# Performance work log

Measured on AMD Instinct MI355X. Metric: run time of the kernel, lower is better.

The kernel has to match this reference:

```python
import jax, jax.numpy as jnp
import numpy as np

N, E = 40000, 640000
IN_DIM, EDGE_DIM, HID = 128, 64, 128


def setup_inputs() -> dict:
    key = jax.random.key(0)
    ks = jax.random.split(key, 10)
    x = jax.random.normal(ks[0], (N, IN_DIM), dtype=jnp.float32)
    edge_index = jax.random.randint(ks[1], (2, E), 0, N, dtype=jnp.int64)
    edge_attr = jax.random.normal(ks[2], (E, EDGE_DIM), dtype=jnp.float32)
    # learned params (xavier-ish scaling)
    Wh_w = jax.random.normal(ks[3], (EDGE_DIM, HID), dtype=jnp.float32) / np.sqrt(EDGE_DIM)
    Wh_b = jnp.zeros((HID,), dtype=jnp.float32)
    Wn_w = jax.random.normal(ks[4], (2 * IN_DIM, HID), dtype=jnp.float32) / np.sqrt(2 * IN_DIM)
    Wn_b = jnp.zeros((HID,), dtype=jnp.float32)
    w_e = jax.random.normal(ks[5], (HID, 1), dtype=jnp.float32) / np.sqrt(HID)
    ft_w = jax.random.normal(ks[6], (IN_DIM, IN_DIM), dtype=jnp.float32) / np.sqrt(IN_DIM)
    ft_b = jnp.zeros((IN_DIM,), dtype=jnp.float32)
    return {"x": x, "edge_index": edge_index, "edge_attr": edge_attr,
            "Wh_w": Wh_w, "Wh_b": Wh_b, "Wn_w": Wn_w, "Wn_b": Wn_b,
            "w_e": w_e, "ft_w": ft_w, "ft_b": ft_b}


def reference(x, edge_index, edge_attr, Wh_w, Wh_b, Wn_w, Wn_b, w_e, ft_w, ft_b):
    src, dst = edge_index[0], edge_index[1]
    # gather endpoint features and run edge MLP: relu(W_h(e) + W_n([x_src; x_dst]))
    node_feat = jnp.concatenate([x[src], x[dst]], axis=1)          # [E, 2*in_dim]
    edge_h = edge_attr @ Wh_w + Wh_b                               # [E, hid]
    node_h = node_feat @ Wn_w + Wn_b                               # [E, hid]
    combined = jax.nn.relu(edge_h + node_h)
    scores = (combined @ w_e)[:, 0]                                # [E]
    alpha = jax.nn.softmax(scores, axis=0)                         # softmax over all edges
    # scatter-add weighted dst features into src nodes (same-type branch)
    local = jnp.zeros_like(x).at[src].add(-alpha[:, None] * x[dst])
    out = x + local
    out = out + out @ ft_w + ft_b
    return out
```

## Files before the change

### kernel.cpp

```cpp
#include <hip/hip_runtime.h>
#include <math.h>

#define N_NODES 40000
#define E_EDGES 640000
#define IN_DIM 128
#define EDGE_DIM 64
#define HID 128
#define EB 10000

typedef unsigned int u32;
typedef unsigned short u16;
typedef __attribute__((ext_vector_type(4))) float f32x4;
typedef __attribute__((ext_vector_type(8))) short bf16x8;

__device__ __forceinline__ float bf_lo(u32 d) { return __uint_as_float(d << 16); }
__device__ __forceinline__ float bf_hi(u32 d) { return __uint_as_float(d & 0xffff0000u); }
__device__ __forceinline__ u16 f2bf(float f) {
    u32 u = __float_as_uint(f);
    return (u16)((u + 0x7fffu + ((u >> 16) & 1u)) >> 16);
}
__device__ __forceinline__ u32 pack_bf(float lo, float hi) {
    return ((u32)f2bf(hi) << 16) | (u32)f2bf(lo);
}


__global__ __launch_bounds__(256) void k_init(const float* __restrict__ x,
                                              u16* __restrict__ xb,
                                              u32* __restrict__ counts) {
    int i = blockIdx.x * 256 + threadIdx.x;
    xb[i] = f2bf(x[i]);
    if (i < N_NODES) counts[i] = 0;
}

__global__ __launch_bounds__(256) void k_trans(const float* __restrict__ Whw,
                                               const float* __restrict__ Wnw,
                                               const float* __restrict__ ftw,
                                               u16* __restrict__ Whtb,
                                               u16* __restrict__ WnAT,
                                               u16* __restrict__ WnBT,
                                               u16* __restrict__ fttb) {
    int i = blockIdx.x * 256 + threadIdx.x;
    if (i < 8192) {
        int h = i >> 6, k = i & 63;
        Whtb[i] = f2bf(Whw[k * HID + h]);
    } else if (i < 24576) {
        int j = i - 8192, h = j >> 7, k = j & 127;
        WnAT[j] = f2bf(Wnw[k * HID + h]);
    } else if (i < 40960) {
        int j = i - 24576, h = j >> 7, k = j & 127;
        WnBT[j] = f2bf(Wnw[(IN_DIM + k) * HID + h]);
    } else {
        int j = i - 40960, h = j >> 7, k = j & 127;
        fttb[j] = f2bf(ftw[k * IN_DIM + h]);
    }
}

__global__ __launch_bounds__(256) void k_proj(const u16* __restrict__ xb,
                                              const u16* __restrict__ WnAT,
                                              const u16* __restrict__ WnBT,
                                              const float* __restrict__ Whb,
                                              const float* __restrict__ Wnb,
                                              u16* __restrict__ P1b,
                                              u16* __restrict__ P2b) {
    const int t = threadIdx.x, w = t >> 6, lane = t & 63;
    const int mrow = lane & 15, quad = lane >> 4;
    const int rowBase = blockIdx.x * 64 + w * 16;

    bf16x8 a[4];
    const u16* ar = xb + (size_t)(rowBase + mrow) * IN_DIM + quad * 8;
#pragma unroll
    for (int ks = 0; ks < 4; ++ks) a[ks] = *(const bf16x8*)(ar + ks * 32);

#pragma unroll
    for (int nt = 0; nt < 8; ++nt) {
        const u16* b1p = WnAT + (size_t)(nt * 16 + mrow) * IN_DIM + quad * 8;
        const u16* b2p = WnBT + (size_t)(nt * 16 + mrow) * IN_DIM + quad * 8;
        f32x4 c1 = {0.f, 0.f, 0.f, 0.f}, c2 = {0.f, 0.f, 0.f, 0.f};
#pragma unroll
        for (int ks = 0; ks < 4; ++ks) {
            c1 = __builtin_amdgcn_mfma_f32_16x16x32_bf16(a[ks], *(const bf16x8*)(b1p + ks * 32), c1, 0, 0, 0);
            c2 = __builtin_amdgcn_mfma_f32_16x16x32_bf16(a[ks], *(const bf16x8*)(b2p + ks * 32), c2, 0, 0, 0);
        }
        const int col = nt * 16 + mrow;
        const float bias = Whb[col] + Wnb[col];
#pragma unroll
        for (int r = 0; r < 4; ++r) {
            int row = rowBase + quad * 4 + r;
            P1b[(size_t)row * HID + col] = f2bf(c1[r] + bias);
            P2b[(size_t)row * HID + col] = f2bf(c2[r]);
        }
    }
}

__global__ __launch_bounds__(256) void k_hist(const int* __restrict__ eidx,
                                              u32* __restrict__ counts) {
    int e = blockIdx.x * 256 + threadIdx.x;
    atomicAdd(&counts[eidx[e]], 1u);
}

__global__ __launch_bounds__(1024) void k_scan(const u32* __restrict__ counts,
                                               u32* __restrict__ off,
                                               u32* __restrict__ cur) {
    __shared__ u32 sums[1024];
    const int t = threadIdx.x;
    const int CH = 40;
    u32 local[CH];
    u32 s = 0;
    const int base = t * CH;
#pragma unroll
    for (int i = 0; i < CH; ++i) {
        int idx = base + i;
        u32 c = (idx < N_NODES) ? counts[idx] : 0u;
        local[i] = s;
        s += c;
    }
    sums[t] = s;
    __syncthreads();
    for (int o = 1; o < 1024; o <<= 1) {
        u32 v = (t >= o) ? sums[t - o] : 0u;
        __syncthreads();
        sums[t] += v;
        __syncthreads();
    }
    const u32 pre = sums[t] - s;
#pragma unroll
    for (int i = 0; i < CH; ++i) {
        int idx = base + i;
        if (idx < N_NODES) {
            u32 v = pre + local[i];
            off[idx] = v;
            cur[idx] = v;
        }
    }
    if (t == 1023) off[N_NODES] = sums[1023];
}

__global__ __launch_bounds__(256) void k_edge(const int* __restrict__ eidx,
                                              const float* __restrict__ ea,
                                              const u16* __restrict__ Whtb,
                                              const u16* __restrict__ P1b,
                                              const u16* __restrict__ P2b,
                                              const float* __restrict__ we,
                                              float* __restrict__ expS,
                                              float* __restrict__ partials) {
    __shared__ u32 Psp[64][68];
    __shared__ float wsumLds[4];
    const int e0 = blockIdx.x * 64;
    const int t = threadIdx.x;

    {
        const int m = t >> 2, c4 = t & 3;
        int src = eidx[e0 + m];
        int dst = eidx[E_EDGES + e0 + m];
        const uint4* p1 = (const uint4*)(P1b + (size_t)src * HID + c4 * 32);
        const uint4* p2 = (const uint4*)(P2b + (size_t)dst * HID + c4 * 32);
#pragma unroll
        for (int i = 0; i < 4; ++i) {
            uint4 ua = p1[i], ub = p2[i];
            u32 da[4] = {ua.x, ua.y, ua.z, ua.w};
            u32 db[4] = {ub.x, ub.y, ub.z, ub.w};
            uint4 o;
            o.x = pack_bf(bf_lo(da[0]) + bf_lo(db[0]), bf_hi(da[0]) + bf_hi(db[0]));
            o.y = pack_bf(bf_lo(da[1]) + bf_lo(db[1]), bf_hi(da[1]) + bf_hi(db[1]));
            o.z = pack_bf(bf_lo(da[2]) + bf_lo(db[2]), bf_hi(da[2]) + bf_hi(db[2]));
            o.w = pack_bf(bf_lo(da[3]) + bf_lo(db[3]), bf_hi(da[3]) + bf_hi(db[3]));
            *(uint4*)&Psp[m][c4 * 16 + i * 4] = o;
        }
    }
    __syncthreads();

    const int w = t >> 6, lane = t & 63;
    const int mrow = lane & 15, quad = lane >> 4;
    const int mt = w;

    const float* arow = ea + (size_t)(e0 + mt * 16 + mrow) * EDGE_DIM + quad * 8;
    bf16x8 a0, a1;
#pragma unroll
    for (int ks = 0; ks < 2; ++ks) {
        float4 f0 = *(const float4*)(arow + ks * 32);
        float4 f1 = *(const float4*)(arow + ks * 32 + 4);
        bf16x8& af = ks ? a1 : a0;
        af[0] = (short)f2bf(f0.x); af[1] = (short)f2bf(f0.y);
        af[2] = (short)f2bf(f0.z); af[3] = (short)f2bf(f0.w);
        af[4] = (short)f2bf(f1.x); af[5] = (short)f2bf(f1.y);
        af[6] = (short)f2bf(f1.z); af[7] = (short)f2bf(f1.w);
    }

    float wsum[4] = {0.f, 0.f, 0.f, 0.f};
    const u16* bbase = Whtb + (size_t)mrow * EDGE_DIM + quad * 8;
#pragma unroll
    for (int nt = 0; nt < 8; ++nt) {
        const u16* bp = bbase + nt * 16 * EDGE_DIM;
        bf16x8 b0 = *(const bf16x8*)(bp);
        bf16x8 b1 = *(const bf16x8*)(bp + 32);
        f32x4 c = {0.f, 0.f, 0.f, 0.f};
        c = __builtin_amdgcn_mfma_f32_16x16x32_bf16(a0, b0, c, 0, 0, 0);
        c = __builtin_amdgcn_mfma_f32_16x16x32_bf16(a1, b1, c, 0, 0, 0);
        float wv = we[nt * 16 + mrow];
#pragma unroll
        for (int r = 0; r < 4; ++r) {
            u32 u = Psp[mt * 16 + quad * 4 + r][nt * 8 + (mrow >> 1)];
            float p = (mrow & 1) ? bf_hi(u) : bf_lo(u);
            wsum[r] += fmaxf(c[r] + p, 0.f) * wv;
        }
    }

#pragma unroll
    for (int off = 1; off < 16; off <<= 1) {
#pragma unroll
        for (int r = 0; r < 4; ++r) wsum[r] += __shfl_xor(wsum[r], off, 16);
    }
    float ex[4]; float s4 = 0.f;
#pragma unroll
    for (int r = 0; r < 4; ++r) { ex[r] = __expf(wsum[r]); s4 += ex[r]; }
    if (mrow == 0) {
#pragma unroll
        for (int r = 0; r < 4; ++r) expS[e0 + mt * 16 + quad * 4 + r] = ex[r];
    }
    s4 += __shfl_xor(s4, 16, 64);
    s4 += __shfl_xor(s4, 32, 64);
    if (lane == 0) wsumLds[w] = s4;
    __syncthreads();
    if (t == 0) partials[blockIdx.x] = wsumLds[0] + wsumLds[1] + wsumLds[2] + wsumLds[3];
}

__global__ __launch_bounds__(256) void k_sum(const float* __restrict__ partials,
                                             float* __restrict__ sumExp) {
    float s = 0.f;
    for (int i = threadIdx.x; i < EB; i += 256) s += partials[i];
#pragma unroll
    for (int off = 1; off < 64; off <<= 1) s += __shfl_xor(s, off, 64);
    __shared__ float ws4[4];
    if ((threadIdx.x & 63) == 0) ws4[threadIdx.x >> 6] = s;
    __syncthreads();
    if (threadIdx.x == 0) sumExp[0] = ws4[0] + ws4[1] + ws4[2] + ws4[3];
}

__global__ __launch_bounds__(256) void k_fill(const int* __restrict__ eidx,
                                              const float* __restrict__ expS,
                                              const float* __restrict__ sumExp,
                                              u32* __restrict__ cur,
                                              u32* __restrict__ sdst,
                                              float* __restrict__ sa) {
    const float invS = 1.0f / sumExp[0];
    int e = blockIdx.x * 256 + threadIdx.x;
    int src = eidx[e];
    int dst = eidx[E_EDGES + e];
    u32 pos = atomicAdd(&cur[src], 1u);
    sdst[pos] = (u32)dst;
    sa[pos]   = -expS[e] * invS;
}

__global__ __launch_bounds__(256) void k_accum(const u32* __restrict__ off,
                                               const u32* __restrict__ sdst,
                                               const float* __restrict__ sa,
                                               const u16* __restrict__ xb,
                                               float* __restrict__ out) {
    const int lane = threadIdx.x & 63;
    const int n = blockIdx.x * 4 + (threadIdx.x >> 6);
    const u32 o0 = off[n], o1 = off[n + 1];

    float acc0 = 0.f, acc1 = 0.f;
    for (u32 base = o0; base < o1; base += 64) {
        u32 j = base + (u32)lane;
        u32 dv = 0; float av = 0.f;
        if (j < o1) { dv = sdst[j]; av = sa[j]; }
        int cnt = (int)min(64u, o1 - base);
        for (int jj = 0; jj < cnt; ++jj) {
            u32 dst = __shfl(dv, jj, 64);
            float a = __shfl(av, jj, 64);
            u32 d = ((const u32*)(xb + (size_t)dst * IN_DIM))[lane];
            acc0 = fmaf(a, bf_lo(d), acc0);
            acc1 = fmaf(a, bf_hi(d), acc1);
        }
    }
    float* op = out + (size_t)n * IN_DIM + 2 * lane;
    op[0] = acc0;
    op[1] = acc1;
}

__global__ __launch_bounds__(256) void k_final(const float* __restrict__ x,
                                               const u16* __restrict__ fttb,
                                               const float* __restrict__ ftb,
                                               float* __restrict__ out) {
    __shared__ u32 ybp[64][68];
    const int t = threadIdx.x;
    const int rb = blockIdx.x * 64;

    {
        const int rr = t >> 2, seg = t & 3;
        const float4* xp = (const float4*)(x + (size_t)(rb + rr) * IN_DIM + seg * 32);
        const float4* lp = (const float4*)(out + (size_t)(rb + rr) * IN_DIM + seg * 32);
#pragma unroll
        for (int i = 0; i < 4; ++i) {
            float4 xa = xp[2 * i], xc = xp[2 * i + 1];
            float4 la = lp[2 * i], lc = lp[2 * i + 1];
            uint4 o;
            o.x = pack_bf(xa.x + la.x, xa.y + la.y);
            o.y = pack_bf(xa.z + la.z, xa.w + la.w);
            o.z = pack_bf(xc.x + lc.x, xc.y + lc.y);
            o.w = pack_bf(xc.z + lc.z, xc.w + lc.w);
            *(uint4*)&ybp[rr][seg * 16 + i * 4] = o;
        }
    }
    __syncthreads();

    const int w = t >> 6, lane = t & 63;
    const int mrow = lane & 15, quad = lane >> 4;
    const int rowBase = rb + w * 16;

    bf16x8 a[4];
#pragma unroll
    for (int ks = 0; ks < 4; ++ks)
        a[ks] = *(const bf16x8*)&ybp[w * 16 + mrow][ks * 16 + quad * 4];

#pragma unroll
    for (int nt = 0; nt < 8; ++nt) {
        const u16* bp = fttb + (size_t)(nt * 16 + mrow) * IN_DIM + quad * 8;
        f32x4 c = {0.f, 0.f, 0.f, 0.f};
#pragma unroll
        for (int ks = 0; ks < 4; ++ks)
            c = __builtin_amdgcn_mfma_f32_16x16x32_bf16(a[ks], *(const bf16x8*)(bp + ks * 32), c, 0, 0, 0);
        const int col = nt * 16 + mrow;
        const float fb = ftb[col];
#pragma unroll
        for (int r = 0; r < 4; ++r) {
            int row = rowBase + quad * 4 + r;
            size_t idx = (size_t)row * IN_DIM + col;
            float y = x[idx] + out[idx];
            out[idx] = y + c[r] + fb;
        }
    }
}

extern "C" void kernel_launch(void* const* d_in, const int* in_sizes, int n_in,
                              void* d_out, int out_size, void* d_ws, size_t ws_size,
                              hipStream_t stream) {
    const float* x    = (const float*)d_in[0];
    const int*   eidx = (const int*)d_in[1];
    const float* ea   = (const float*)d_in[2];
    const float* Whw  = (const float*)d_in[3];
    const float* Whb  = (const float*)d_in[4];
    const float* Wnw  = (const float*)d_in[5];
    const float* Wnb  = (const float*)d_in[6];
    const float* we   = (const float*)d_in[7];
    const float* ftw  = (const float*)d_in[8];
    const float* ftb  = (const float*)d_in[9];
    float* out = (float*)d_out;

    u16*   P1b      = (u16*)d_ws;
    u16*   P2b      = P1b + (size_t)N_NODES * HID;
    u16*   xb       = P2b + (size_t)N_NODES * HID;
    u16*   Whtb     = xb + (size_t)N_NODES * IN_DIM;
    u16*   WnAT     = Whtb + (size_t)EDGE_DIM * HID;
    u16*   WnBT     = WnAT + (size_t)HID * IN_DIM;
    u16*   fttb     = WnBT + (size_t)HID * IN_DIM;
    float* expS     = (float*)(fttb + (size_t)IN_DIM * IN_DIM);
    float* partials = expS + (size_t)E_EDGES;
    float* sumExp   = partials + EB;
    u32*   counts   = (u32*)(sumExp + 1);
    u32*   off      = counts + N_NODES;
    u32*   cur      = off + N_NODES + 1;
    u32*   sdst     = cur + N_NODES;
    float* sa       = (float*)(sdst + E_EDGES);

    k_init <<<(N_NODES * IN_DIM) / 256, 256, 0, stream>>>(x, xb, counts);
    k_trans<<<224, 256, 0, stream>>>(Whw, Wnw, ftw, Whtb, WnAT, WnBT, fttb);
    k_proj <<<N_NODES / 64, 256, 0, stream>>>(xb, WnAT, WnBT, Whb, Wnb, P1b, P2b);
    k_hist <<<E_EDGES / 256, 256, 0, stream>>>(eidx, counts);
    k_scan <<<1, 1024, 0, stream>>>(counts, off, cur);
    k_edge <<<EB, 256, 0, stream>>>(eidx, ea, Whtb, P1b, P2b, we, expS, partials);
    k_sum  <<<1, 256, 0, stream>>>(partials, sumExp);
    k_fill <<<E_EDGES / 256, 256, 0, stream>>>(eidx, expS, sumExp, cur, sdst, sa);
    k_accum<<<N_NODES / 4, 256, 0, stream>>>(off, sdst, sa, xb, out);
    k_final<<<N_NODES / 64, 256, 0, stream>>>(x, fttb, ftb, out);
}
```

Measured before the change: 570.3 us.

## Fuse CSR fill into edge kernel and defer softmax normalization to accumulation

The CSR bucket fill (atomic slot reservation plus writing dst and the unnormalized negative exp score) moves into the edge-score kernel, and the separate fill kernel and expS buffer are removed. Normalization by the global exp sum is applied once per output element in the accumulation kernel. The edge kernel drops its block-wide syncs by giving each wave its own LDS tile and per-wave partial sums, and it issues the gathers and edge_attr loads together before computing. The accumulation loop is unrolled by four with packed (dst, weight) pairs so that more gathers are in flight. In exchange, atomics now run inside the MFMA kernel, which may serialize on hot nodes and add latency there.

```diff
diff --git a/kernel.cpp b/kernel.cpp
--- a/kernel.cpp
+++ b/kernel.cpp
@@ -7,6 +7,7 @@
 #define EDGE_DIM 64
 #define HID 128
 #define EB 10000
+#define NPART (EB * 4)
 
 typedef unsigned int u32;
 typedef unsigned short u16;
@@ -141,50 +142,50 @@
                                               const u16* __restrict__ P1b,
                                               const u16* __restrict__ P2b,
                                               const float* __restrict__ we,
-                                              float* __restrict__ expS,
+                                              u32* __restrict__ cur,
+                                              uint2* __restrict__ sde,
                                               float* __restrict__ partials) {
-    __shared__ u32 Psp[64][68];
-    __shared__ float wsumLds[4];
-    const int e0 = blockIdx.x * 64;
-    const int t = threadIdx.x;
-
-    {
-        const int m = t >> 2, c4 = t & 3;
-        int src = eidx[e0 + m];
-        int dst = eidx[E_EDGES + e0 + m];
-        const uint4* p1 = (const uint4*)(P1b + (size_t)src * HID + c4 * 32);
-        const uint4* p2 = (const uint4*)(P2b + (size_t)dst * HID + c4 * 32);
-#pragma unroll
-        for (int i = 0; i < 4; ++i) {
-            uint4 ua = p1[i], ub = p2[i];
-            u32 da[4] = {ua.x, ua.y, ua.z, ua.w};
-            u32 db[4] = {ub.x, ub.y, ub.z, ub.w};
-            uint4 o;
-            o.x = pack_bf(bf_lo(da[0]) + bf_lo(db[0]), bf_hi(da[0]) + bf_hi(db[0]));
-            o.y = pack_bf(bf_lo(da[1]) + bf_lo(db[1]), bf_hi(da[1]) + bf_hi(db[1]));
-            o.z = pack_bf(bf_lo(da[2]) + bf_lo(db[2]), bf_hi(da[2]) + bf_hi(db[2]));
-            o.w = pack_bf(bf_lo(da[3]) + bf_lo(db[3]), bf_hi(da[3]) + bf_hi(db[3]));
-            *(uint4*)&Psp[m][c4 * 16 + i * 4] = o;
-        }
-    }
-    __syncthreads();
-
-    const int w = t >> 6, lane = t & 63;
+    __shared__ u32 Psp[4][16][68];
+    const int t = threadIdx.x, w = t >> 6, lane = t & 63;
+    const int e0 = blockIdx.x * 64 + w * 16;
     const int mrow = lane & 15, quad = lane >> 4;
-    const int mt = w;
-
-    const float* arow = ea + (size_t)(e0 + mt * 16 + mrow) * EDGE_DIM + quad * 8;
+
+    const int m = lane >> 2, c4 = lane & 3;
+    const int srcm = eidx[e0 + m];
+    const int dstm = eidx[E_EDGES + e0 + m];
+    const uint4* p1 = (const uint4*)(P1b + (size_t)srcm * HID + c4 * 32);
+    const uint4* p2 = (const uint4*)(P2b + (size_t)dstm * HID + c4 * 32);
+    uint4 pa[4], pb[4];
+#pragma unroll
+    for (int i = 0; i < 4; ++i) { pa[i] = p1[i]; pb[i] = p2[i]; }
+
+    const float* arow = ea + (size_t)(e0 + mrow) * EDGE_DIM + quad * 8;
+    float4 f0 = *(const float4*)(arow);
+    float4 f1 = *(const float4*)(arow + 4);
+    float4 f2 = *(const float4*)(arow + 32);
+    float4 f3 = *(const float4*)(arow + 36);
+
+#pragma unroll
+    for (int i = 0; i < 4; ++i) {
+        u32 da[4] = {pa[i].x, pa[i].y, pa[i].z, pa[i].w};
+        u32 db[4] = {pb[i].x, pb[i].y, pb[i].z, pb[i].w};
+        uint4 o;
+        o.x = pack_bf(bf_lo(da[0]) + bf_lo(db[0]), bf_hi(da[0]) + bf_hi(db[0]));
+        o.y = pack_bf(bf_lo(da[1]) + bf_lo(db[1]), bf_hi(da[1]) + bf_hi(db[1]));
+        o.z = pack_bf(bf_lo(da[2]) + bf_lo(db[2]), bf_hi(da[2]) + bf_hi(db[2]));
+        o.w = pack_bf(bf_lo(da[3]) + bf_lo(db[3]), bf_hi(da[3]) + bf_hi(db[3]));
+        *(uint4*)&Psp[w][m][c4 * 16 + i * 4] = o;
+    }
+
     bf16x8 a0, a1;
-#pragma unroll
-    for (int ks = 0; ks < 2; ++ks) {
-        float4 f0 = *(const float4*)(arow + ks * 32);
-        float4 f1 = *(const float4*)(arow + ks * 32 + 4);
-        bf16x8& af = ks ? a1 : a0;
-        af[0] = (short)f2bf(f0.x); af[1] = (short)f2bf(f0.y);
-        af[2] = (short)f2bf(f0.z); af[3] = (short)f2bf(f0.w);
-        af[4] = (short)f2bf(f1.x); af[5] = (short)f2bf(f1.y);
-        af[6] = (short)f2bf(f1.z); af[7] = (short)f2bf(f1.w);
-    }
+    a0[0] = (short)f2bf(f0.x); a0[1] = (short)f2bf(f0.y);
+    a0[2] = (short)f2bf(f0.z); a0[3] = (short)f2bf(f0.w);
+    a0[4] = (short)f2bf(f1.x); a0[5] = (short)f2bf(f1.y);
+    a0[6] = (short)f2bf(f1.z); a0[7] = (short)f2bf(f1.w);
+    a1[0] = (short)f2bf(f2.x); a1[1] = (short)f2bf(f2.y);
+    a1[2] = (short)f2bf(f2.z); a1[3] = (short)f2bf(f2.w);
+    a1[4] = (short)f2bf(f3.x); a1[5] = (short)f2bf(f3.y);
+    a1[6] = (short)f2bf(f3.z); a1[7] = (short)f2bf(f3.w);
 
     float wsum[4] = {0.f, 0.f, 0.f, 0.f};
     const u16* bbase = Whtb + (size_t)mrow * EDGE_DIM + quad * 8;
@@ -199,7 +200,7 @@
         float wv = we[nt * 16 + mrow];
 #pragma unroll
         for (int r = 0; r < 4; ++r) {
-            u32 u = Psp[mt * 16 + quad * 4 + r][nt * 8 + (mrow >> 1)];
+            u32 u = Psp[w][quad * 4 + r][nt * 8 + (mrow >> 1)];
             float p = (mrow & 1) ? bf_hi(u) : bf_lo(u);
             wsum[r] += fmaxf(c[r] + p, 0.f) * wv;
         }
@@ -213,21 +214,27 @@
     float ex[4]; float s4 = 0.f;
 #pragma unroll
     for (int r = 0; r < 4; ++r) { ex[r] = __expf(wsum[r]); s4 += ex[r]; }
+
     if (mrow == 0) {
 #pragma unroll
-        for (int r = 0; r < 4; ++r) expS[e0 + mt * 16 + quad * 4 + r] = ex[r];
-    }
+        for (int r = 0; r < 4; ++r) {
+            int e = e0 + quad * 4 + r;
+            int s = eidx[e];
+            int d = eidx[E_EDGES + e];
+            u32 pos = atomicAdd(&cur[s], 1u);
+            sde[pos] = make_uint2((u32)d, __float_as_uint(-ex[r]));
+        }
+    }
+
     s4 += __shfl_xor(s4, 16, 64);
     s4 += __shfl_xor(s4, 32, 64);
-    if (lane == 0) wsumLds[w] = s4;
-    __syncthreads();
-    if (t == 0) partials[blockIdx.x] = wsumLds[0] + wsumLds[1] + wsumLds[2] + wsumLds[3];
+    if (lane == 0) partials[blockIdx.x * 4 + w] = s4;
 }
 
 __global__ __launch_bounds__(256) void k_sum(const float* __restrict__ partials,
                                              float* __restrict__ sumExp) {
     float s = 0.f;
-    for (int i = threadIdx.x; i < EB; i += 256) s += partials[i];
+    for (int i = threadIdx.x; i < NPART; i += 256) s += partials[i];
 #pragma unroll
     for (int off = 1; off < 64; off <<= 1) s += __shfl_xor(s, off, 64);
     __shared__ float ws4[4];
@@ -236,26 +243,12 @@
     if (threadIdx.x == 0) sumExp[0] = ws4[0] + ws4[1] + ws4[2] + ws4[3];
 }
 
-__global__ __launch_bounds__(256) void k_fill(const int* __restrict__ eidx,
-                                              const float* __restrict__ expS,
-                                              const float* __restrict__ sumExp,
-                                              u32* __restrict__ cur,
-                                              u32* __restrict__ sdst,
-                                              float* __restrict__ sa) {
-    const float invS = 1.0f / sumExp[0];
-    int e = blockIdx.x * 256 + threadIdx.x;
-    int src = eidx[e];
-    int dst = eidx[E_EDGES + e];
-    u32 pos = atomicAdd(&cur[src], 1u);
-    sdst[pos] = (u32)dst;
-    sa[pos]   = -expS[e] * invS;
-}
-
 __global__ __launch_bounds__(256) void k_accum(const u32* __restrict__ off,
-                                               const u32* __restrict__ sdst,
-                                               const float* __restrict__ sa,
+                                               const uint2* __restrict__ sde,
+                                               const float* __restrict__ sumExp,
                                                const u16* __restrict__ xb,
                                                float* __restrict__ out) {
+    const float invS = 1.0f / sumExp[0];
     const int lane = threadIdx.x & 63;
     const int n = blockIdx.x * 4 + (threadIdx.x >> 6);
     const u32 o0 = off[n], o1 = off[n + 1];
@@ -263,20 +256,37 @@
     float acc0 = 0.f, acc1 = 0.f;
     for (u32 base = o0; base < o1; base += 64) {
         u32 j = base + (u32)lane;
-        u32 dv = 0; float av = 0.f;
-        if (j < o1) { dv = sdst[j]; av = sa[j]; }
+        uint2 dv = make_uint2(0u, 0u);
+        if (j < o1) dv = sde[j];
         int cnt = (int)min(64u, o1 - base);
-        for (int jj = 0; jj < cnt; ++jj) {
-            u32 dst = __shfl(dv, jj, 64);
-            float a = __shfl(av, jj, 64);
-            u32 d = ((const u32*)(xb + (size_t)dst * IN_DIM))[lane];
-            acc0 = fmaf(a, bf_lo(d), acc0);
-            acc1 = fmaf(a, bf_hi(d), acc1);
+        int jj = 0;
+        for (; jj + 4 <= cnt; jj += 4) {
+            u32 d0 = __shfl(dv.x, jj, 64),     d1 = __shfl(dv.x, jj + 1, 64);
+            u32 d2 = __shfl(dv.x, jj + 2, 64), d3 = __shfl(dv.x, jj + 3, 64);
+            float a0 = __uint_as_float(__shfl(dv.y, jj, 64));
+            float a1 = __uint_as_float(__shfl(dv.y, jj + 1, 64));
+            float a2 = __uint_as_float(__shfl(dv.y, jj + 2, 64));
+            float a3 = __uint_as_float(__shfl(dv.y, jj + 3, 64));
+            u32 q0 = ((const u32*)(xb + (size_t)d0 * IN_DIM))[lane];
+            u32 q1 = ((const u32*)(xb + (size_t)d1 * IN_DIM))[lane];
+            u32 q2 = ((const u32*)(xb + (size_t)d2 * IN_DIM))[lane];
+            u32 q3 = ((const u32*)(xb + (size_t)d3 * IN_DIM))[lane];
+            acc0 = fmaf(a0, bf_lo(q0), acc0); acc1 = fmaf(a0, bf_hi(q0), acc1);
+            acc0 = fmaf(a1, bf_lo(q1), acc0); acc1 = fmaf(a1, bf_hi(q1), acc1);
+            acc0 = fmaf(a2, bf_lo(q2), acc0); acc1 = fmaf(a2, bf_hi(q2), acc1);
+            acc0 = fmaf(a3, bf_lo(q3), acc0); acc1 = fmaf(a3, bf_hi(q3), acc1);
+        }
+        for (; jj < cnt; ++jj) {
+            u32 dst = __shfl(dv.x, jj, 64);
+            float a = __uint_as_float(__shfl(dv.y, jj, 64));
+            u32 q = ((const u32*)(xb + (size_t)dst * IN_DIM))[lane];
+            acc0 = fmaf(a, bf_lo(q), acc0);
+            acc1 = fmaf(a, bf_hi(q), acc1);
         }
     }
     float* op = out + (size_t)n * IN_DIM + 2 * lane;
-    op[0] = acc0;
-    op[1] = acc1;
+    op[0] = acc0 * invS;
+    op[1] = acc1 * invS;
 }
 
 __global__ __launch_bounds__(256) void k_final(const float* __restrict__ x,
@@ -348,30 +358,27 @@
     const float* ftb  = (const float*)d_in[9];
     float* out = (float*)d_out;
 
-    u16*   P1b      = (u16*)d_ws;
+    uint2* sde      = (uint2*)d_ws;
+    u16*   P1b      = (u16*)(sde + (size_t)E_EDGES);
     u16*   P2b      = P1b + (size_t)N_NODES * HID;
     u16*   xb       = P2b + (size_t)N_NODES * HID;
     u16*   Whtb     = xb + (size_t)N_NODES * IN_DIM;
     u16*   WnAT     = Whtb + (size_t)EDGE_DIM * HID;
     u16*   WnBT     = WnAT + (size_t)HID * IN_DIM;
     u16*   fttb     = WnBT + (size_t)HID * IN_DIM;
-    float* expS     = (float*)(fttb + (size_t)IN_DIM * IN_DIM);
-    float* partials = expS + (size_t)E_EDGES;
-    float* sumExp   = partials + EB;
+    float* partials = (float*)(fttb + (size_t)IN_DIM * IN_DIM);
+    float* sumExp   = partials + NPART;
     u32*   counts   = (u32*)(sumExp + 1);
     u32*   off      = counts + N_NODES;
     u32*   cur      = off + N_NODES + 1;
-    u32*   sdst     = cur + N_NODES;
-    float* sa       = (float*)(sdst + E_EDGES);
 
     k_init <<<(N_NODES * IN_DIM) / 256, 256, 0, stream>>>(x, xb, counts);
     k_trans<<<224, 256, 0, stream>>>(Whw, Wnw, ftw, Whtb, WnAT, WnBT, fttb);
     k_proj <<<N_NODES / 64, 256, 0, stream>>>(xb, WnAT, WnBT, Whb, Wnb, P1b, P2b);
     k_hist <<<E_EDGES / 256, 256, 0, stream>>>(eidx, counts);
     k_scan <<<1, 1024, 0, stream>>>(counts, off, cur);
-    k_edge <<<EB, 256, 0, stream>>>(eidx, ea, Whtb, P1b, P2b, we, expS, partials);
+    k_edge <<<EB, 256, 0, stream>>>(eidx, ea, Whtb, P1b, P2b, we, cur, sde, partials);
     k_sum  <<<1, 256, 0, stream>>>(partials, sumExp);
-    k_fill <<<E_EDGES / 256, 256, 0, stream>>>(eidx, expS, sumExp, cur, sdst, sa);
-    k_accum<<<N_NODES / 4, 256, 0, stream>>>(off, sdst, sa, xb, out);
+    k_accum<<<N_NODES / 4, 256, 0, stream>>>(off, sde, sumExp, xb, out);
     k_final<<<N_NODES / 64, 256, 0, stream>>>(x, fttb, ftb, out);
 }
```

After: 565.4 us. Within noise of the previous version (-0.9%).
